# Performance work log

Hardware: AMD Instinct MI355X
Metric: run time of the kernel (lower is better)

The kernel has to match this reference:

```python
import jax, jax.numpy as jnp
import numpy as np

N_IN = 512
SCALE = 0  # s / n_in**scale == s when scale=0

def setup_inputs() -> dict:
    key = jax.random.key(0)
    k1, k2, k3, k4 = jax.random.split(key, 4)
    B, S, D = 4, 128, N_IN
    x = jax.random.normal(k1, (B, S, D), dtype=jnp.float32)
    y = jax.random.normal(k2, (B, S, D), dtype=jnp.float32)
    z = jax.random.normal(k3, (B, S, D), dtype=jnp.float32)
    # weight: (n_out, n_in + bias_x, n_in, n_in + bias_y)
    weight = jax.random.normal(k4, (1, D + 1, D, D + 1), dtype=jnp.float32) * 0.02
    return {"x": x, "y": y, "z": z, "weight": weight}

def reference(x, y, z, weight):
    # append bias-1 column to x and y (bias_x=bias_y=True)
    ones = jnp.ones_like(x[..., :1])
    xb = jnp.concatenate([x, ones], axis=-1)           # [b, s, n_in+1]
    yb = jnp.concatenate([y, jnp.ones_like(y[..., :1])], axis=-1)
    # w = z^T W : [b, o, z, i, j]
    w = jnp.einsum('bzk,oikj->bozij', z, weight)
    # s(x,y,z) = x^T (z^T W) y : [b, o, z, x, y]
    s = jnp.einsum('bxi,bozij,byj->bozxy', xb, w, yb)
    # n_out == 1 -> squeeze channel dim; scale == 0 -> divide by n_in**0 == 1
    return jnp.squeeze(s, axis=1) / (N_IN ** SCALE)
```

## Files before the change

kernel.cpp:

```cpp
#include <hip/hip_runtime.h>
#include <stdint.h>


typedef __attribute__((ext_vector_type(8))) short bf16x8;
typedef __attribute__((ext_vector_type(4))) float f32x4;

__device__ __forceinline__ unsigned short f2bf(float f) {
    unsigned int u = __float_as_uint(f);
    u += 0x7fffu + ((u >> 16) & 1u);
    return (unsigned short)(u >> 16);
}

__device__ __forceinline__ void gload_lds16(const void* g, void* l) {
    __builtin_amdgcn_global_load_lds((const __attribute__((address_space(1))) void*)g,
                                     (__attribute__((address_space(3))) void*)l, 16, 0, 0);
}

__global__ __launch_bounds__(256) void k_cast(const float* __restrict__ x,
    const float* __restrict__ y, const float* __restrict__ z,
    unsigned short* __restrict__ xbf, unsigned short* __restrict__ ybf,
    unsigned short* __restrict__ zbf)
{
    int t = blockIdx.x * 256 + threadIdx.x;
    int arr = t >> 15;
    int off = (t & 32767) * 8;
    const float* src = (arr == 0) ? x : (arr == 1) ? y : z;
    unsigned short* dst = (arr == 0) ? xbf : (arr == 1) ? ybf : zbf;
    float4 a = *(const float4*)(src + off);
    float4 b = *(const float4*)(src + off + 4);
    uint4 o;
    o.x = f2bf(a.x) | ((unsigned)f2bf(a.y) << 16);
    o.y = f2bf(a.z) | ((unsigned)f2bf(a.w) << 16);
    o.z = f2bf(b.x) | ((unsigned)f2bf(b.y) << 16);
    o.w = f2bf(b.z) | ((unsigned)f2bf(b.w) << 16);
    *(uint4*)(dst + off) = o;
}

__global__ __launch_bounds__(256) void k_edge(const float* __restrict__ z,
    const float* __restrict__ w, float* __restrict__ a_arr,
    float* __restrict__ c_arr, float* __restrict__ d_arr)
{
    __shared__ float Zs[64][33];
    __shared__ float Bs[32][65];
    int t = threadIdx.x;
    int mb = blockIdx.x % 17, bzb = blockIdx.x / 17;
    int tr = t >> 4, tc = t & 15;
    float acc[4][4] = {};
    for (int k0 = 0; k0 < 512; k0 += 32) {
        __syncthreads();
        {   int row = t >> 2, ko = (t & 3) * 8;
            const float* p = z + (bzb * 64 + row) * 512 + k0 + ko;
            float4 v0 = ((const float4*)p)[0], v1 = ((const float4*)p)[1];
            Zs[row][ko + 0] = v0.x; Zs[row][ko + 1] = v0.y; Zs[row][ko + 2] = v0.z; Zs[row][ko + 3] = v0.w;
            Zs[row][ko + 4] = v1.x; Zs[row][ko + 5] = v1.y; Zs[row][ko + 6] = v1.z; Zs[row][ko + 7] = v1.w;
        }
        {   int kr = t >> 3, mo = (t & 7) * 8;
            for (int e = 0; e < 8; ++e) {
                int m = mb * 64 + mo + e;
                float v = 0.f;
                int krow = k0 + kr;
                if (m < 512)        v = w[(m * 512 + krow) * 513 + 512];
                else if (m < 1024)  v = w[(262144 + krow) * 513 + (m - 512)];
                else if (m == 1024) v = w[(262144 + krow) * 513 + 512];
                Bs[kr][mo + e] = v;
            }
        }
        __syncthreads();
        for (int kk = 0; kk < 32; ++kk) {
            float zr[4], br[4];
            for (int r = 0; r < 4; ++r) zr[r] = Zs[tr * 4 + r][kk];
            for (int c = 0; c < 4; ++c) br[c] = Bs[kk][tc * 4 + c];
            for (int r = 0; r < 4; ++r)
                for (int c = 0; c < 4; ++c) acc[r][c] += zr[r] * br[c];
        }
    }
    for (int r = 0; r < 4; ++r)
        for (int c = 0; c < 4; ++c) {
            int bz = bzb * 64 + tr * 4 + r;
            int m = mb * 64 + tc * 4 + c;
            if (m < 512)        a_arr[bz * 512 + m] = acc[r][c];
            else if (m < 1024)  c_arr[bz * 512 + (m - 512)] = acc[r][c];
            else if (m == 1024) d_arr[bz] = acc[r][c];
        }
}

__global__ __launch_bounds__(512, 2) void k_gemm1(const unsigned short* __restrict__ zbf,
    const float* __restrict__ w, unsigned short* __restrict__ Mws)
{
    extern __shared__ unsigned char smem[];
    unsigned char* Zb0 = smem;
    unsigned char* Zb1 = smem + 32768;
    unsigned char* Bb0 = smem + 65536;
    unsigned char* Bb1 = smem + 73728;

    int nwg = gridDim.x, cpx = nwg >> 3;
    int bid = blockIdx.x;
    int swz = (bid & 7) * cpx + (bid >> 3);
    int iloc = swz >> 2, jb = swz & 3;
    int j0 = jb * 128;
    int t = threadIdx.x, wid = t >> 6, lane = t & 63;
    int bzg = wid >> 1, jg = wid & 1;
    int l15 = lane & 15, l4 = lane >> 4;

    int arow = lane >> 2;
    int akc  = (lane & 3) ^ ((lane >> 3) & 3);
    const unsigned short* zbase = zbf + (size_t)(wid * 64 + arow) * 512 + akc * 8;

    int jB = t & 127, kq8 = t >> 7;
    const float* wb = w + (size_t)iloc * 262656 + (size_t)(kq8 * 8) * 513 + j0 + jB;
    int bwoff = jB * 64 + ((kq8 ^ ((jB >> 1) & 3)) * 16);

    int aoff = (bzg * 128 + l15) * 64 + ((l4 ^ ((l15 >> 1) & 3)) * 16);
    int boff = (jg * 64 + l15) * 64 + ((l4 ^ ((l15 >> 1) & 3)) * 16);

    f32x4 acc[8][4];
    #pragma unroll
    for (int mt = 0; mt < 8; ++mt)
        #pragma unroll
        for (int nt = 0; nt < 4; ++nt) acc[mt][nt] = (f32x4){0.f, 0.f, 0.f, 0.f};

    float wr[2][8];

    #pragma unroll
    for (int q = 0; q < 4; ++q)
        gload_lds16(zbase + q * 8192, Zb0 + wid * 4096 + q * 1024);
    {
        #pragma unroll
        for (int e = 0; e < 8; ++e) wr[0][e] = __builtin_nontemporal_load(wb + (size_t)e * 513);
        const float* wp = wb + (size_t)32 * 513;
        #pragma unroll
        for (int e = 0; e < 8; ++e) wr[1][e] = __builtin_nontemporal_load(wp + (size_t)e * 513);
        uint4 pk;
        pk.x = f2bf(wr[0][0]) | ((unsigned)f2bf(wr[0][1]) << 16);
        pk.y = f2bf(wr[0][2]) | ((unsigned)f2bf(wr[0][3]) << 16);
        pk.z = f2bf(wr[0][4]) | ((unsigned)f2bf(wr[0][5]) << 16);
        pk.w = f2bf(wr[0][6]) | ((unsigned)f2bf(wr[0][7]) << 16);
        *(uint4*)(Bb0 + bwoff) = pk;
    }
    asm volatile("s_waitcnt lgkmcnt(0)" ::: "memory");
    __builtin_amdgcn_s_barrier();
    __builtin_amdgcn_sched_barrier(0);

    #pragma unroll
    for (int ks = 0; ks < 16; ++ks) {
        const int cur = ks & 1;
        unsigned char* Zcur  = cur ? Zb1 : Zb0;
        unsigned char* Znext = cur ? Zb0 : Zb1;
        unsigned char* Bcur  = cur ? Bb1 : Bb0;
        unsigned char* Bnext = cur ? Bb0 : Bb1;

        if (ks < 15) {
            #pragma unroll
            for (int q = 0; q < 4; ++q)
                gload_lds16(zbase + (ks + 1) * 32 + q * 8192, Znext + wid * 4096 + q * 1024);
        }
        if (ks < 14) {
            const float* wp = wb + (size_t)(ks + 2) * 32 * 513;
            #pragma unroll
            for (int e = 0; e < 8; ++e) wr[cur][e] = __builtin_nontemporal_load(wp + (size_t)e * 513);
        }
        bf16x8 bfr[4];
        #pragma unroll
        for (int nt = 0; nt < 4; ++nt)
            bfr[nt] = *(const bf16x8*)(Bcur + boff + nt * 1024);
        #pragma unroll
        for (int mt = 0; mt < 8; ++mt) {
            bf16x8 afr = *(const bf16x8*)(Zcur + aoff + mt * 1024);
            #pragma unroll
            for (int nt = 0; nt < 4; ++nt)
                acc[mt][nt] = __builtin_amdgcn_mfma_f32_16x16x32_bf16(afr, bfr[nt], acc[mt][nt], 0, 0, 0);
        }
        if (ks < 15) {
            uint4 pk;
            pk.x = f2bf(wr[cur ^ 1][0]) | ((unsigned)f2bf(wr[cur ^ 1][1]) << 16);
            pk.y = f2bf(wr[cur ^ 1][2]) | ((unsigned)f2bf(wr[cur ^ 1][3]) << 16);
            pk.z = f2bf(wr[cur ^ 1][4]) | ((unsigned)f2bf(wr[cur ^ 1][5]) << 16);
            pk.w = f2bf(wr[cur ^ 1][6]) | ((unsigned)f2bf(wr[cur ^ 1][7]) << 16);
            *(uint4*)(Bnext + bwoff) = pk;
        }
        if (ks < 14) {
            asm volatile("s_waitcnt vmcnt(8) lgkmcnt(0)" ::: "memory");
        } else if (ks == 14) {
            asm volatile("s_waitcnt vmcnt(0) lgkmcnt(0)" ::: "memory");
        }
        if (ks < 15) {
            __builtin_amdgcn_s_barrier();
            __builtin_amdgcn_sched_barrier(0);
        }
    }

    #pragma unroll
    for (int mt = 0; mt < 8; ++mt)
        #pragma unroll
        for (int nt = 0; nt < 4; ++nt)
            #pragma unroll
            for (int r = 0; r < 4; ++r) {
                int bz = bzg * 128 + mt * 16 + l4 * 4 + r;
                int j  = j0 + jg * 64 + nt * 16 + l15;
                Mws[(size_t)bz * 262144 + (size_t)iloc * 512 + j] = f2bf(acc[mt][nt][r]);
            }
}

__global__ __launch_bounds__(512, 2) void k_fuse(const unsigned short* __restrict__ xbf,
    const unsigned short* __restrict__ ybf, const unsigned short* __restrict__ Mws,
    const float* __restrict__ xf, const float* __restrict__ yf,
    const float* __restrict__ a_arr, const float* __restrict__ c_arr,
    const float* __restrict__ d_arr, float* __restrict__ out)
{
    extern __shared__ unsigned char smem[];
    __shared__ float part[512];
    __shared__ float uv[256];

    int bid = blockIdx.x;
    int bz = (bid & 7) * 64 + (bid >> 3);
    int b = bz >> 7;
    int t = threadIdx.x, wid = t >> 6, lane = t & 63;
    int l15 = lane & 15, l4 = lane >> 4;
    int xg = wid >> 2, yg = wid & 3;
    int g8 = wid;

    const unsigned short* ybase = ybf + (size_t)(b * 128) * 512;
    #pragma unroll
    for (int it = 0; it < 16; ++it) {
        int row = it * 8 + wid;
        gload_lds16(ybase + (size_t)row * 512 + ((lane ^ (row & 63)) * 8),
                    smem + it * 8192 + t * 16);
    }

    {
        int xr = t & 127, q = t >> 7;
        {   const float* xp = xf + (size_t)(b * 128 + xr) * 512 + q * 128;
            const float* ap = a_arr + bz * 512 + q * 128;
            float s = 0.f;
            for (int ii = 0; ii < 128; ++ii) s += xp[ii] * ap[ii];
            part[q * 128 + xr] = s;
        }
        __syncthreads();
        if (t < 128) uv[t] = part[t] + part[128 + t] + part[256 + t] + part[384 + t];
        __syncthreads();
        {   const float* yp = yf + (size_t)(b * 128 + xr) * 512 + q * 128;
            const float* cp = c_arr + bz * 512 + q * 128;
            float s = 0.f;
            for (int ii = 0; ii < 128; ++ii) s += yp[ii] * cp[ii];
            part[q * 128 + xr] = s;
        }
        __syncthreads();
        if (t < 128) uv[128 + t] = part[t] + part[128 + t] + part[256 + t] + part[384 + t];
        __syncthreads();
    }

    const unsigned short* mbase = Mws + (size_t)bz * 262144
                                + (size_t)(g8 * 64 + l15) * 512 + l4 * 8;
    f32x4 accR[4][8];
    #pragma unroll
    for (int mt = 0; mt < 4; ++mt)
        #pragma unroll
        for (int nt = 0; nt < 8; ++nt) accR[mt][nt] = (f32x4){0.f, 0.f, 0.f, 0.f};

    bf16x8 mfr[4][4];
    #pragma unroll
    for (int d = 0; d < 4; ++d)
        #pragma unroll
        for (int mt = 0; mt < 4; ++mt)
            mfr[d][mt] = *(const bf16x8*)(mbase + (size_t)mt * 8192 + d * 32);

    #pragma unroll
    for (int kf = 0; kf < 16; ++kf) {
        #pragma unroll
        for (int nh = 0; nh < 2; ++nh) {
            bf16x8 yfr[4];
            #pragma unroll
            for (int n4 = 0; n4 < 4; ++n4) {
                int y = (nh * 4 + n4) * 16 + l15;
                yfr[n4] = *(const bf16x8*)(smem + y * 1024 + (((kf * 4 + l4) ^ (y & 63)) * 16));
            }
            #pragma unroll
            for (int mt = 0; mt < 4; ++mt)
                #pragma unroll
                for (int n4 = 0; n4 < 4; ++n4)
                    accR[mt][nh * 4 + n4] = __builtin_amdgcn_mfma_f32_16x16x32_bf16(
                        mfr[kf & 3][mt], yfr[n4], accR[mt][nh * 4 + n4], 0, 0, 0);
        }
        if (kf < 12) {
            #pragma unroll
            for (int mt = 0; mt < 4; ++mt)
                mfr[kf & 3][mt] = *(const bf16x8*)(mbase + (size_t)mt * 8192 + (kf + 4) * 32);
        }
    }
    asm volatile("s_waitcnt lgkmcnt(0)" ::: "memory");
    __builtin_amdgcn_s_barrier();
    __builtin_amdgcn_sched_barrier(0);

    #pragma unroll
    for (int mt = 0; mt < 4; ++mt)
        #pragma unroll
        for (int nt = 0; nt < 8; ++nt) {
            int y = nt * 16 + l15;
            int chunk = g8 * 8 + mt * 2 + (l4 >> 1);
            int byte = y * 1024 + ((chunk ^ (y & 63)) * 16) + (l4 & 1) * 8;
            unsigned p0 = f2bf(accR[mt][nt][0]) | ((unsigned)f2bf(accR[mt][nt][1]) << 16);
            unsigned p1 = f2bf(accR[mt][nt][2]) | ((unsigned)f2bf(accR[mt][nt][3]) << 16);
            *(uint2*)(smem + byte) = make_uint2(p0, p1);
        }
    asm volatile("s_waitcnt lgkmcnt(0)" ::: "memory");
    __builtin_amdgcn_s_barrier();
    __builtin_amdgcn_sched_barrier(0);

    float dv = d_arr[bz];
    f32x4 acc[4][2];
    #pragma unroll
    for (int mt = 0; mt < 4; ++mt)
        #pragma unroll
        for (int nt = 0; nt < 2; ++nt) {
            int y = yg * 32 + nt * 16 + l15;
            #pragma unroll
            for (int r = 0; r < 4; ++r) {
                int x = xg * 64 + mt * 16 + l4 * 4 + r;
                acc[mt][nt][r] = uv[x] + uv[128 + y] + dv;
            }
        }

    const unsigned short* xbase = xbf + (size_t)(b * 128 + xg * 64 + l15) * 512 + l4 * 8;
    bf16x8 xfr[3][4];
    #pragma unroll
    for (int d = 0; d < 3; ++d)
        #pragma unroll
        for (int mt = 0; mt < 4; ++mt)
            xfr[d][mt] = *(const bf16x8*)(xbase + (size_t)mt * 8192 + d * 32);

    #pragma unroll
    for (int kf = 0; kf < 16; ++kf) {
        bf16x8 rfr[2];
        #pragma unroll
        for (int nt = 0; nt < 2; ++nt) {
            int y = yg * 32 + nt * 16 + l15;
            rfr[nt] = *(const bf16x8*)(smem + y * 1024 + (((kf * 4 + l4) ^ (y & 63)) * 16));
        }
        #pragma unroll
        for (int mt = 0; mt < 4; ++mt)
            #pragma unroll
            for (int nt = 0; nt < 2; ++nt)
                acc[mt][nt] = __builtin_amdgcn_mfma_f32_16x16x32_bf16(
                    xfr[kf % 3][mt], rfr[nt], acc[mt][nt], 0, 0, 0);
        if (kf < 13) {
            #pragma unroll
            for (int mt = 0; mt < 4; ++mt)
                xfr[kf % 3][mt] = *(const bf16x8*)(xbase + (size_t)mt * 8192 + (kf + 3) * 32);
        }
    }

    float* op = out + (size_t)bz * 16384;
    #pragma unroll
    for (int mt = 0; mt < 4; ++mt)
        #pragma unroll
        for (int nt = 0; nt < 2; ++nt)
            #pragma unroll
            for (int r = 0; r < 4; ++r) {
                int x = xg * 64 + mt * 16 + l4 * 4 + r;
                int y = yg * 32 + nt * 16 + l15;
                op[x * 128 + y] = acc[mt][nt][r];
            }
}

extern "C" void kernel_launch(void* const* d_in, const int* in_sizes, int n_in,
                              void* d_out, int out_size, void* d_ws, size_t ws_size,
                              hipStream_t stream)
{
    const float* x = (const float*)d_in[0];
    const float* y = (const float*)d_in[1];
    const float* z = (const float*)d_in[2];
    const float* w = (const float*)d_in[3];
    float* out = (float*)d_out;
    char* ws = (char*)d_ws;

    unsigned short* xbf = (unsigned short*)(ws + 0);
    unsigned short* ybf = (unsigned short*)(ws + 524288);
    unsigned short* zbf = (unsigned short*)(ws + 1048576);
    float* a_arr = (float*)(ws + 1572864);
    float* c_arr = (float*)(ws + 2621440);
    float* d_arr = (float*)(ws + 3670016);
    unsigned short* Mws = (unsigned short*)(ws + 3674112);

    hipLaunchKernelGGL(k_cast, dim3(384), dim3(256), 0, stream, x, y, z, xbf, ybf, zbf);
    hipLaunchKernelGGL(k_edge, dim3(136), dim3(256), 0, stream, z, w, a_arr, c_arr, d_arr);
    hipLaunchKernelGGL(k_gemm1, dim3(2048), dim3(512), 81920, stream, zbf, w, Mws);
    hipLaunchKernelGGL(k_fuse, dim3(512), dim3(512), 131072, stream, xbf, ybf, Mws,
                       x, y, a_arr, c_arr, d_arr, out);
}
```

Before: 461.3 us.

## Split fused kernel into separate uv, M·Y and X·R kernels with LDS double buffering

```diff
diff --git a/kernel.cpp b/kernel.cpp
--- a/kernel.cpp
+++ b/kernel.cpp
@@ -84,6 +84,48 @@
         }
 }
 
+__global__ __launch_bounds__(512) void k_uv(const float* __restrict__ xf,
+    const float* __restrict__ yf, const float* __restrict__ a_arr,
+    const float* __restrict__ c_arr, float* __restrict__ u_arr,
+    float* __restrict__ v_arr)
+{
+    __shared__ float part[512];
+    int bz = blockIdx.x;
+    int b = bz >> 7;
+    int t = threadIdx.x, r = t >> 2, q = t & 3;
+    {
+        const float* xp = xf + (size_t)(b * 128 + r) * 512;
+        const float* ap = a_arr + bz * 512;
+        float s = 0.f;
+        #pragma unroll 4
+        for (int c0 = 0; c0 < 32; ++c0) {
+            int col = c0 * 16 + q * 4;
+            float4 xv = *(const float4*)(xp + col);
+            float4 av = *(const float4*)(ap + col);
+            s += xv.x * av.x + xv.y * av.y + xv.z * av.z + xv.w * av.w;
+        }
+        part[t] = s;
+    }
+    __syncthreads();
+    if (t < 128) u_arr[bz * 128 + t] = part[t*4] + part[t*4+1] + part[t*4+2] + part[t*4+3];
+    __syncthreads();
+    {
+        const float* yp = yf + (size_t)(b * 128 + r) * 512;
+        const float* cp = c_arr + bz * 512;
+        float s = 0.f;
+        #pragma unroll 4
+        for (int c0 = 0; c0 < 32; ++c0) {
+            int col = c0 * 16 + q * 4;
+            float4 yv = *(const float4*)(yp + col);
+            float4 cv = *(const float4*)(cp + col);
+            s += yv.x * cv.x + yv.y * cv.y + yv.z * cv.z + yv.w * cv.w;
+        }
+        part[t] = s;
+    }
+    __syncthreads();
+    if (t < 128) v_arr[bz * 128 + t] = part[t*4] + part[t*4+1] + part[t*4+2] + part[t*4+3];
+}
+
 __global__ __launch_bounds__(512, 2) void k_gemm1(const unsigned short* __restrict__ zbf,
     const float* __restrict__ w, unsigned short* __restrict__ Mws)
 {
@@ -201,165 +243,155 @@
             }
 }
 
-__global__ __launch_bounds__(512, 2) void k_fuse(const unsigned short* __restrict__ xbf,
-    const unsigned short* __restrict__ ybf, const unsigned short* __restrict__ Mws,
-    const float* __restrict__ xf, const float* __restrict__ yf,
-    const float* __restrict__ a_arr, const float* __restrict__ c_arr,
-    const float* __restrict__ d_arr, float* __restrict__ out)
-{
-    extern __shared__ unsigned char smem[];
-    __shared__ float part[512];
-    __shared__ float uv[256];
-
+__global__ __launch_bounds__(512, 4) void k_p2(const unsigned short* __restrict__ Mws,
+    const unsigned short* __restrict__ ybf, unsigned short* __restrict__ Rws)
+{
+    __shared__ unsigned char Mt[2][8192];
+    __shared__ unsigned char Yt[2][8192];
+    int bid = blockIdx.x;
+    int swz = (bid & 7) * 256 + (bid >> 3);
+    int bz = swz >> 2, ib = swz & 3;
+    int b = bz >> 7;
+    int t = threadIdx.x, wid = t >> 6, lane = t & 63;
+    int l15 = lane & 15, l4 = lane >> 4;
+    int ig = wid >> 1, yg = wid & 1;
+
+    int srow = t >> 2;
+    int sch  = (t & 3) ^ (srow & 3);
+    const unsigned short* msrc = Mws + (size_t)bz * 262144 + (size_t)(ib * 128 + srow) * 512 + sch * 8;
+    const unsigned short* ysrc = ybf + (size_t)(b * 128 + srow) * 512 + sch * 8;
+
+    f32x4 acc[2][4];
+    #pragma unroll
+    for (int mt = 0; mt < 2; ++mt)
+        #pragma unroll
+        for (int nt = 0; nt < 4; ++nt) acc[mt][nt] = (f32x4){0.f, 0.f, 0.f, 0.f};
+
+    gload_lds16(msrc, &Mt[0][t * 16]);
+    gload_lds16(ysrc, &Yt[0][t * 16]);
+    asm volatile("s_waitcnt vmcnt(0)" ::: "memory");
+    __builtin_amdgcn_s_barrier();
+    __builtin_amdgcn_sched_barrier(0);
+
+    #pragma unroll
+    for (int ks = 0; ks < 16; ++ks) {
+        const int cur = ks & 1;
+        if (ks < 15) {
+            gload_lds16(msrc + (ks + 1) * 32, &Mt[cur ^ 1][t * 16]);
+            gload_lds16(ysrc + (ks + 1) * 32, &Yt[cur ^ 1][t * 16]);
+        }
+        bf16x8 afr[2], bfr[4];
+        #pragma unroll
+        for (int mt = 0; mt < 2; ++mt) {
+            int r2 = ig * 32 + mt * 16 + l15;
+            afr[mt] = *(const bf16x8*)(&Mt[cur][r2 * 64 + ((l4 ^ (r2 & 3)) * 16)]);
+        }
+        #pragma unroll
+        for (int nt = 0; nt < 4; ++nt) {
+            int r2 = yg * 64 + nt * 16 + l15;
+            bfr[nt] = *(const bf16x8*)(&Yt[cur][r2 * 64 + ((l4 ^ (r2 & 3)) * 16)]);
+        }
+        #pragma unroll
+        for (int mt = 0; mt < 2; ++mt)
+            #pragma unroll
+            for (int nt = 0; nt < 4; ++nt)
+                acc[mt][nt] = __builtin_amdgcn_mfma_f32_16x16x32_bf16(afr[mt], bfr[nt], acc[mt][nt], 0, 0, 0);
+        if (ks < 15) {
+            asm volatile("s_waitcnt vmcnt(0)" ::: "memory");
+            __builtin_amdgcn_s_barrier();
+            __builtin_amdgcn_sched_barrier(0);
+        }
+    }
+
+    #pragma unroll
+    for (int mt = 0; mt < 2; ++mt)
+        #pragma unroll
+        for (int nt = 0; nt < 4; ++nt) {
+            int y = yg * 64 + nt * 16 + l15;
+            int i = ib * 128 + ig * 32 + mt * 16 + l4 * 4;
+            unsigned p0 = f2bf(acc[mt][nt][0]) | ((unsigned)f2bf(acc[mt][nt][1]) << 16);
+            unsigned p1 = f2bf(acc[mt][nt][2]) | ((unsigned)f2bf(acc[mt][nt][3]) << 16);
+            *(uint2*)(Rws + (size_t)bz * 65536 + (size_t)y * 512 + i) = make_uint2(p0, p1);
+        }
+}
+
+__global__ __launch_bounds__(512, 4) void k_p3(const unsigned short* __restrict__ xbf,
+    const unsigned short* __restrict__ Rws, const float* __restrict__ u_arr,
+    const float* __restrict__ v_arr, const float* __restrict__ d_arr,
+    float* __restrict__ out)
+{
+    __shared__ unsigned char Xt[2][8192];
+    __shared__ unsigned char Rt[2][8192];
     int bid = blockIdx.x;
     int bz = (bid & 7) * 64 + (bid >> 3);
     int b = bz >> 7;
     int t = threadIdx.x, wid = t >> 6, lane = t & 63;
     int l15 = lane & 15, l4 = lane >> 4;
     int xg = wid >> 2, yg = wid & 3;
-    int g8 = wid;
-
-    const unsigned short* ybase = ybf + (size_t)(b * 128) * 512;
-    #pragma unroll
-    for (int it = 0; it < 16; ++it) {
-        int row = it * 8 + wid;
-        gload_lds16(ybase + (size_t)row * 512 + ((lane ^ (row & 63)) * 8),
-                    smem + it * 8192 + t * 16);
-    }
-
-    {
-        int xr = t & 127, q = t >> 7;
-        {   const float* xp = xf + (size_t)(b * 128 + xr) * 512 + q * 128;
-            const float* ap = a_arr + bz * 512 + q * 128;
-            float s = 0.f;
-            for (int ii = 0; ii < 128; ++ii) s += xp[ii] * ap[ii];
-            part[q * 128 + xr] = s;
-        }
-        __syncthreads();
-        if (t < 128) uv[t] = part[t] + part[128 + t] + part[256 + t] + part[384 + t];
-        __syncthreads();
-        {   const float* yp = yf + (size_t)(b * 128 + xr) * 512 + q * 128;
-            const float* cp = c_arr + bz * 512 + q * 128;
-            float s = 0.f;
-            for (int ii = 0; ii < 128; ++ii) s += yp[ii] * cp[ii];
-            part[q * 128 + xr] = s;
-        }
-        __syncthreads();
-        if (t < 128) uv[128 + t] = part[t] + part[128 + t] + part[256 + t] + part[384 + t];
-        __syncthreads();
-    }
-
-    const unsigned short* mbase = Mws + (size_t)bz * 262144
-                                + (size_t)(g8 * 64 + l15) * 512 + l4 * 8;
-    f32x4 accR[4][8];
+
+    int srow = t >> 2;
+    int sch  = (t & 3) ^ (srow & 3);
+    const unsigned short* xsrc = xbf + (size_t)(b * 128 + srow) * 512 + sch * 8;
+    const unsigned short* rsrc = Rws + (size_t)bz * 65536 + (size_t)srow * 512 + sch * 8;
+
+    f32x4 acc[4][2];
     #pragma unroll
     for (int mt = 0; mt < 4; ++mt)
         #pragma unroll
-        for (int nt = 0; nt < 8; ++nt) accR[mt][nt] = (f32x4){0.f, 0.f, 0.f, 0.f};
-
-    bf16x8 mfr[4][4];
-    #pragma unroll
-    for (int d = 0; d < 4; ++d)
-        #pragma unroll
-        for (int mt = 0; mt < 4; ++mt)
-            mfr[d][mt] = *(const bf16x8*)(mbase + (size_t)mt * 8192 + d * 32);
-
-    #pragma unroll
-    for (int kf = 0; kf < 16; ++kf) {
-        #pragma unroll
-        for (int nh = 0; nh < 2; ++nh) {
-            bf16x8 yfr[4];
-            #pragma unroll
-            for (int n4 = 0; n4 < 4; ++n4) {
-                int y = (nh * 4 + n4) * 16 + l15;
-                yfr[n4] = *(const bf16x8*)(smem + y * 1024 + (((kf * 4 + l4) ^ (y & 63)) * 16));
-            }
-            #pragma unroll
-            for (int mt = 0; mt < 4; ++mt)
-                #pragma unroll
-                for (int n4 = 0; n4 < 4; ++n4)
-                    accR[mt][nh * 4 + n4] = __builtin_amdgcn_mfma_f32_16x16x32_bf16(
-                        mfr[kf & 3][mt], yfr[n4], accR[mt][nh * 4 + n4], 0, 0, 0);
-        }
-        if (kf < 12) {
-            #pragma unroll
-            for (int mt = 0; mt < 4; ++mt)
-                mfr[kf & 3][mt] = *(const bf16x8*)(mbase + (size_t)mt * 8192 + (kf + 4) * 32);
-        }
-    }
-    asm volatile("s_waitcnt lgkmcnt(0)" ::: "memory");
+        for (int nt = 0; nt < 2; ++nt) acc[mt][nt] = (f32x4){0.f, 0.f, 0.f, 0.f};
+
+    gload_lds16(xsrc, &Xt[0][t * 16]);
+    gload_lds16(rsrc, &Rt[0][t * 16]);
+    asm volatile("s_waitcnt vmcnt(0)" ::: "memory");
     __builtin_amdgcn_s_barrier();
     __builtin_amdgcn_sched_barrier(0);
 
     #pragma unroll
-    for (int mt = 0; mt < 4; ++mt)
-        #pragma unroll
-        for (int nt = 0; nt < 8; ++nt) {
-            int y = nt * 16 + l15;
-            int chunk = g8 * 8 + mt * 2 + (l4 >> 1);
-            int byte = y * 1024 + ((chunk ^ (y & 63)) * 16) + (l4 & 1) * 8;
-            unsigned p0 = f2bf(accR[mt][nt][0]) | ((unsigned)f2bf(accR[mt][nt][1]) << 16);
-            unsigned p1 = f2bf(accR[mt][nt][2]) | ((unsigned)f2bf(accR[mt][nt][3]) << 16);
-            *(uint2*)(smem + byte) = make_uint2(p0, p1);
-        }
-    asm volatile("s_waitcnt lgkmcnt(0)" ::: "memory");
-    __builtin_amdgcn_s_barrier();
-    __builtin_amdgcn_sched_barrier(0);
+    for (int ks = 0; ks < 16; ++ks) {
+        const int cur = ks & 1;
+        if (ks < 15) {
+            gload_lds16(xsrc + (ks + 1) * 32, &Xt[cur ^ 1][t * 16]);
+            gload_lds16(rsrc + (ks + 1) * 32, &Rt[cur ^ 1][t * 16]);
+        }
+        bf16x8 afr[4], bfr[2];
+        #pragma unroll
+        for (int mt = 0; mt < 4; ++mt) {
+            int r2 = xg * 64 + mt * 16 + l15;
+            afr[mt] = *(const bf16x8*)(&Xt[cur][r2 * 64 + ((l4 ^ (r2 & 3)) * 16)]);
+        }
+        #pragma unroll
+        for (int nt = 0; nt < 2; ++nt) {
+            int r2 = yg * 32 + nt * 16 + l15;
+            bfr[nt] = *(const bf16x8*)(&Rt[cur][r2 * 64 + ((l4 ^ (r2 & 3)) * 16)]);
+        }
+        #pragma unroll
+        for (int mt = 0; mt < 4; ++mt)
+            #pragma unroll
+            for (int nt = 0; nt < 2; ++nt)
+                acc[mt][nt] = __builtin_amdgcn_mfma_f32_16x16x32_bf16(afr[mt], bfr[nt], acc[mt][nt], 0, 0, 0);
+        if (ks < 15) {
+            asm volatile("s_waitcnt vmcnt(0)" ::: "memory");
+            __builtin_amdgcn_s_barrier();
+            __builtin_amdgcn_sched_barrier(0);
+        }
+    }
 
     float dv = d_arr[bz];
-    f32x4 acc[4][2];
-    #pragma unroll
-    for (int mt = 0; mt < 4; ++mt)
+    float* op = out + (size_t)bz * 16384;
+    #pragma unroll
+    for (int mt = 0; mt < 4; ++mt) {
+        float4 uq = *(const float4*)(u_arr + bz * 128 + xg * 64 + mt * 16 + l4 * 4);
         #pragma unroll
         for (int nt = 0; nt < 2; ++nt) {
             int y = yg * 32 + nt * 16 + l15;
-            #pragma unroll
-            for (int r = 0; r < 4; ++r) {
-                int x = xg * 64 + mt * 16 + l4 * 4 + r;
-                acc[mt][nt][r] = uv[x] + uv[128 + y] + dv;
-            }
-        }
-
-    const unsigned short* xbase = xbf + (size_t)(b * 128 + xg * 64 + l15) * 512 + l4 * 8;
-    bf16x8 xfr[3][4];
-    #pragma unroll
-    for (int d = 0; d < 3; ++d)
-        #pragma unroll
-        for (int mt = 0; mt < 4; ++mt)
-            xfr[d][mt] = *(const bf16x8*)(xbase + (size_t)mt * 8192 + d * 32);
-
-    #pragma unroll
-    for (int kf = 0; kf < 16; ++kf) {
-        bf16x8 rfr[2];
-        #pragma unroll
-        for (int nt = 0; nt < 2; ++nt) {
-            int y = yg * 32 + nt * 16 + l15;
-            rfr[nt] = *(const bf16x8*)(smem + y * 1024 + (((kf * 4 + l4) ^ (y & 63)) * 16));
-        }
-        #pragma unroll
-        for (int mt = 0; mt < 4; ++mt)
-            #pragma unroll
-            for (int nt = 0; nt < 2; ++nt)
-                acc[mt][nt] = __builtin_amdgcn_mfma_f32_16x16x32_bf16(
-                    xfr[kf % 3][mt], rfr[nt], acc[mt][nt], 0, 0, 0);
-        if (kf < 13) {
-            #pragma unroll
-            for (int mt = 0; mt < 4; ++mt)
-                xfr[kf % 3][mt] = *(const bf16x8*)(xbase + (size_t)mt * 8192 + (kf + 3) * 32);
-        }
-    }
-
-    float* op = out + (size_t)bz * 16384;
-    #pragma unroll
-    for (int mt = 0; mt < 4; ++mt)
-        #pragma unroll
-        for (int nt = 0; nt < 2; ++nt)
-            #pragma unroll
-            for (int r = 0; r < 4; ++r) {
-                int x = xg * 64 + mt * 16 + l4 * 4 + r;
-                int y = yg * 32 + nt * 16 + l15;
-                op[x * 128 + y] = acc[mt][nt][r];
-            }
+            float vv = v_arr[bz * 128 + y] + dv;
+            int x0 = xg * 64 + mt * 16 + l4 * 4;
+            op[(x0 + 0) * 128 + y] = acc[mt][nt][0] + uq.x + vv;
+            op[(x0 + 1) * 128 + y] = acc[mt][nt][1] + uq.y + vv;
+            op[(x0 + 2) * 128 + y] = acc[mt][nt][2] + uq.z + vv;
+            op[(x0 + 3) * 128 + y] = acc[mt][nt][3] + uq.w + vv;
+        }
+    }
 }
 
 extern "C" void kernel_launch(void* const* d_in, const int* in_sizes, int n_in,
@@ -373,17 +405,21 @@
     float* out = (float*)d_out;
     char* ws = (char*)d_ws;
 
-    unsigned short* xbf = (unsigned short*)(ws + 0);
-    unsigned short* ybf = (unsigned short*)(ws + 524288);
-    unsigned short* zbf = (unsigned short*)(ws + 1048576);
+    unsigned short* xbf  = (unsigned short*)(ws + 0);
+    unsigned short* ybf  = (unsigned short*)(ws + 524288);
+    unsigned short* zbf  = (unsigned short*)(ws + 1048576);
     float* a_arr = (float*)(ws + 1572864);
     float* c_arr = (float*)(ws + 2621440);
     float* d_arr = (float*)(ws + 3670016);
-    unsigned short* Mws = (unsigned short*)(ws + 3674112);
+    float* u_arr = (float*)(ws + 3674112);
+    float* v_arr = (float*)(ws + 3936256);
+    unsigned short* Mws = (unsigned short*)(ws + 4198400);
+    unsigned short* Rws = (unsigned short*)(ws + 272633856);
 
     hipLaunchKernelGGL(k_cast, dim3(384), dim3(256), 0, stream, x, y, z, xbf, ybf, zbf);
     hipLaunchKernelGGL(k_edge, dim3(136), dim3(256), 0, stream, z, w, a_arr, c_arr, d_arr);
+    hipLaunchKernelGGL(k_uv, dim3(512), dim3(512), 0, stream, x, y, a_arr, c_arr, u_arr, v_arr);
     hipLaunchKernelGGL(k_gemm1, dim3(2048), dim3(512), 81920, stream, zbf, w, Mws);
-    hipLaunchKernelGGL(k_fuse, dim3(512), dim3(512), 131072, stream, xbf, ybf, Mws,
-                       x, y, a_arr, c_arr, d_arr, out);
-}
+    hipLaunchKernelGGL(k_p2, dim3(2048), dim3(512), 0, stream, Mws, ybf, Rws);
+    hipLaunchKernelGGL(k_p3, dim3(512), dim3(512), 0, stream, xbf, Rws, u_arr, v_arr, d_arr, out);
+}
```

Result: slower. 486.0 us (+5.4%).

## Split MFMA loop into two phases with barriers and priority raise

Applied to the files above, without the earlier changes.

```diff
diff --git a/kernel.cpp b/kernel.cpp
--- a/kernel.cpp
+++ b/kernel.cpp
@@ -163,13 +163,27 @@
         #pragma unroll
         for (int nt = 0; nt < 4; ++nt)
             bfr[nt] = *(const bf16x8*)(Bcur + boff + nt * 1024);
-        #pragma unroll
-        for (int mt = 0; mt < 8; ++mt) {
-            bf16x8 afr = *(const bf16x8*)(Zcur + aoff + mt * 1024);
+        bf16x8 afr0[4];
+        #pragma unroll
+        for (int mt = 0; mt < 4; ++mt)
+            afr0[mt] = *(const bf16x8*)(Zcur + aoff + mt * 1024);
+        __builtin_amdgcn_s_barrier();
+        asm volatile("s_waitcnt lgkmcnt(0)" ::: "memory");
+        __builtin_amdgcn_sched_barrier(0);
+        __builtin_amdgcn_s_setprio(1);
+        #pragma unroll
+        for (int mt = 0; mt < 4; ++mt)
             #pragma unroll
             for (int nt = 0; nt < 4; ++nt)
-                acc[mt][nt] = __builtin_amdgcn_mfma_f32_16x16x32_bf16(afr, bfr[nt], acc[mt][nt], 0, 0, 0);
-        }
+                acc[mt][nt] = __builtin_amdgcn_mfma_f32_16x16x32_bf16(afr0[mt], bfr[nt], acc[mt][nt], 0, 0, 0);
+        __builtin_amdgcn_s_setprio(0);
+        __builtin_amdgcn_s_barrier();
+        __builtin_amdgcn_sched_barrier(0);
+
+        bf16x8 afr1[4];
+        #pragma unroll
+        for (int mt = 0; mt < 4; ++mt)
+            afr1[mt] = *(const bf16x8*)(Zcur + aoff + (mt + 4) * 1024);
         if (ks < 15) {
             uint4 pk;
             pk.x = f2bf(wr[cur ^ 1][0]) | ((unsigned)f2bf(wr[cur ^ 1][1]) << 16);
@@ -182,11 +196,20 @@
             asm volatile("s_waitcnt vmcnt(8) lgkmcnt(0)" ::: "memory");
         } else if (ks == 14) {
             asm volatile("s_waitcnt vmcnt(0) lgkmcnt(0)" ::: "memory");
+        } else {
+            asm volatile("s_waitcnt lgkmcnt(0)" ::: "memory");
         }
         if (ks < 15) {
             __builtin_amdgcn_s_barrier();
             __builtin_amdgcn_sched_barrier(0);
         }
+        __builtin_amdgcn_s_setprio(1);
+        #pragma unroll
+        for (int mt = 0; mt < 4; ++mt)
+            #pragma unroll
+            for (int nt = 0; nt < 4; ++nt)
+                acc[mt + 4][nt] = __builtin_amdgcn_mfma_f32_16x16x32_bf16(afr1[mt], bfr[nt], acc[mt + 4][nt], 0, 0, 0);
+        __builtin_amdgcn_s_setprio(0);
     }
 
     #pragma unroll
```

Result: slower. 491.3 us (+6.5%).
